# Kernel optimization log

Hardware: AMD Instinct MI355X
Metric: run time of the kernel (lower is better)

The kernel has to match this reference:

```python
import jax, jax.numpy as jnp
import numpy as np

N, D, H, E = 8192, 1024, 4096, 8


def setup_inputs() -> dict:
    key = jax.random.key(0)
    ks = jax.random.split(key, 5)
    s_in = 1.0 / np.sqrt(D)
    s_h = 1.0 / np.sqrt(H)
    return {
        "x": jax.random.normal(ks[0], (N, D), dtype=jnp.float32),
        "Wg": jax.random.normal(ks[1], (D, E), dtype=jnp.float32) * s_in,
        "bg": jnp.zeros((E,), dtype=jnp.float32),
        "W1": jax.random.normal(ks[2], (E, D, H), dtype=jnp.float32) * s_in,
        "b1": jnp.zeros((E, H), dtype=jnp.float32),
        "W2": jax.random.normal(ks[3], (E, H, D), dtype=jnp.float32) * s_h,
        "b2": jnp.zeros((E, D), dtype=jnp.float32),
    }


def reference(x, Wg, bg, W1, b1, W2, b2):
    # gate: softmax linear router -> weights [N, E]
    weights = jax.nn.softmax(x @ Wg + bg, axis=-1)
    # all experts, batched GEMMs: h [N, E, H]
    h = jax.nn.relu(jnp.einsum("nd,edh->neh", x, W1) + b1)  # Dropout is identity at inference
    outputs = jnp.einsum("neh,ehd->ned", h, W2) + b2         # [N, E, D]
    # weighted combine over experts
    return jnp.einsum("ne,ned->nd", weights, outputs)
```

## Files before the change

kernel.cpp:

```cpp
#include <hip/hip_runtime.h>
#include <hip/hip_bf16.h>

#define DDIM 1024
#define HDIM 4096
#define NEXP 8
#define NROW 8192

typedef __attribute__((ext_vector_type(8))) short s16x8;
typedef __attribute__((ext_vector_type(4))) float f32x4;

using bf16 = __hip_bfloat16;

__device__ __forceinline__ void gload16(const bf16* g, bf16* lds) {
    __builtin_amdgcn_global_load_lds(
        (const __attribute__((address_space(1))) unsigned int*)g,
        (__attribute__((address_space(3))) unsigned int*)lds,
        16, 0, 0);
}

template <int N>
__device__ __forceinline__ void wait_vmcnt() {
    if constexpr (N >= 6)      asm volatile("s_waitcnt vmcnt(6)" ::: "memory");
    else if constexpr (N == 3) asm volatile("s_waitcnt vmcnt(3)" ::: "memory");
    else                       asm volatile("s_waitcnt vmcnt(0)" ::: "memory");
}

__global__ void cvt_x_kernel(const float* __restrict__ x, bf16* __restrict__ xb, int total4) {
    int i = blockIdx.x * 256 + threadIdx.x;
    if (i >= total4) return;
    float4 v = ((const float4*)x)[i];
    union { bf16 b[4]; uint2 u; } p;
    p.b[0] = __float2bfloat16(v.x);
    p.b[1] = __float2bfloat16(v.y);
    p.b[2] = __float2bfloat16(v.z);
    p.b[3] = __float2bfloat16(v.w);
    ((uint2*)xb)[i] = p.u;
}

__global__ void transpose_cvt_kernel(const float* __restrict__ in, bf16* __restrict__ out,
                                     int R, int C) {
    __shared__ float tile[32][33];
    const size_t esz = (size_t)R * C;
    const float* src = in + (size_t)blockIdx.z * esz;
    bf16* dst = out + (size_t)blockIdx.z * esz;
    int c0 = blockIdx.x * 32, r0 = blockIdx.y * 32;
    int tx = threadIdx.x & 31, ty = threadIdx.x >> 5;
#pragma unroll
    for (int i = 0; i < 32; i += 8)
        tile[ty + i][tx] = src[(size_t)(r0 + ty + i) * C + (c0 + tx)];
    __syncthreads();
#pragma unroll
    for (int i = 0; i < 32; i += 8)
        dst[(size_t)(c0 + ty + i) * R + (r0 + tx)] = __float2bfloat16(tile[tx][ty + i]);
}

__global__ void gate_kernel(const float* __restrict__ x, const float* __restrict__ Wg,
                            const float* __restrict__ bg, float* __restrict__ wts) {
    int wave = threadIdx.x >> 6, lane = threadIdx.x & 63;
    int n = blockIdx.x * 4 + wave;
    const float* xr = x + (size_t)n * DDIM;
    float acc[NEXP] = {0.f, 0.f, 0.f, 0.f, 0.f, 0.f, 0.f, 0.f};
    for (int d = lane; d < DDIM; d += 64) {
        float xv = xr[d];
        const float* wr = Wg + (size_t)d * NEXP;
#pragma unroll
        for (int e = 0; e < NEXP; ++e) acc[e] += xv * wr[e];
    }
#pragma unroll
    for (int off = 32; off > 0; off >>= 1) {
#pragma unroll
        for (int e = 0; e < NEXP; ++e) acc[e] += __shfl_xor(acc[e], off, 64);
    }
    if (lane == 0) {
        float mx = -1e30f;
#pragma unroll
        for (int e = 0; e < NEXP; ++e) { acc[e] += bg[e]; mx = fmaxf(mx, acc[e]); }
        float s = 0.f;
#pragma unroll
        for (int e = 0; e < NEXP; ++e) { acc[e] = __expf(acc[e] - mx); s += acc[e]; }
        float inv = 1.0f / s;
#pragma unroll
        for (int e = 0; e < NEXP; ++e) wts[(size_t)n * NEXP + e] = acc[e] * inv;
    }
}

__global__ void out_init_kernel(const float* __restrict__ wts, const float* __restrict__ b2,
                                float* __restrict__ out) {
    size_t idx = (size_t)blockIdx.x * 256 + threadIdx.x;
    int d = (int)(idx & (DDIM - 1));
    size_t n = idx >> 10;
    const float* w = wts + n * NEXP;
    float s = 0.f;
#pragma unroll
    for (int e = 0; e < NEXP; ++e) s += w[e] * b2[(size_t)e * DDIM + d];
    out[idx] = s;
}

template <int MODE>
__global__ __launch_bounds__(512, 4) void gemm8(
    const bf16* __restrict__ A, const bf16* __restrict__ BT, void* __restrict__ Cout,
    const float* __restrict__ bias, const float* __restrict__ wts,
    int lda, int ldb, int ldc, int NT, int tilesM, int tilesN, int XGN, int expert) {
    constexpr int LPT = 3;
    constexpr int AELEMS = 256 * 32;
    constexpr int BELEMS = 128 * 32;
    __shared__ __align__(16) bf16 lds[3][AELEMS + BELEMS];

    const int tid = threadIdx.x;
    const int wave = tid >> 6, lane = tid & 63;
    const int wm = wave >> 2, wn = wave & 3;
    const int r = lane & 15, kg = lane >> 4;

    const int xcd = blockIdx.x & 7, slot = blockIdx.x >> 3;
    const int XGM = 8 / XGN;
    const int rm = tilesM / XGM, rn = tilesN / XGN;
    const int g = slot >> 5, u = slot & 31;
    const int gpr = rn >> 3;
    const int gm = (g / gpr) * 4 + (u >> 3);
    const int gn = (g % gpr) * 8 + (u & 7);
    const int tm = (xcd / XGN) * rm + gm;
    const int tn = (xcd % XGN) * rn + gn;

    const bf16* gA = A + (size_t)tm * 256 * lda;
    const bf16* gB = BT + (size_t)tn * 128 * ldb;

    f32x4 acc[8][2];
#pragma unroll
    for (int m = 0; m < 8; ++m)
#pragma unroll
        for (int n = 0; n < 2; ++n) acc[m][n] = (f32x4){0.f, 0.f, 0.f, 0.f};

    auto stageA = [&](int t) {
        bf16* Ab = lds[t % 3];
#pragma unroll
        for (int j = 0; j < 2; ++j) {
            int cw = (wave * 2 + j) * 64 + lane;
            int R = cw >> 2, kc = (cw & 3) ^ ((R >> 1) & 3);
            gload16(gA + (size_t)R * lda + t * 32 + kc * 8, Ab + (wave * 2 + j) * 512);
        }
    };
    auto stageB = [&](int t) {
        bf16* Bb = lds[t % 3] + AELEMS;
        int cw = wave * 64 + lane;
        int R = cw >> 2, kc = (cw & 3) ^ ((R >> 1) & 3);
        gload16(gB + (size_t)R * ldb + t * 32 + kc * 8, Bb + wave * 512);
    };

    stageA(0); stageB(0);
    stageA(1); stageB(1);
    wait_vmcnt<LPT>();
    __builtin_amdgcn_s_barrier();

    for (int t = 0; t < NT; ++t) {
        const bf16* Ab = lds[t % 3];
        const bf16* Bb = Ab + AELEMS;
        s16x8 afr[4], bfr[2];

#pragma unroll
        for (int n = 0; n < 2; ++n) {
            int R = wn * 32 + n * 16 + r;
            bfr[n] = *(const s16x8*)(Bb + R * 32 + ((kg ^ ((R >> 1) & 3)) * 8));
        }
#pragma unroll
        for (int m = 0; m < 4; ++m) {
            int R = wm * 128 + m * 16 + r;
            afr[m] = *(const s16x8*)(Ab + R * 32 + ((kg ^ ((R >> 1) & 3)) * 8));
        }
        if (t + 2 < NT) stageA(t + 2);
        __builtin_amdgcn_s_barrier();
        asm volatile("s_waitcnt lgkmcnt(0)" ::: "memory");
        __builtin_amdgcn_sched_barrier(0);
        __builtin_amdgcn_s_setprio(1);
#pragma unroll
        for (int m = 0; m < 4; ++m)
#pragma unroll
            for (int n = 0; n < 2; ++n)
                acc[m][n] = __builtin_amdgcn_mfma_f32_16x16x32_bf16(afr[m], bfr[n], acc[m][n], 0, 0, 0);
        __builtin_amdgcn_s_setprio(0);
        __builtin_amdgcn_s_barrier();

#pragma unroll
        for (int m = 0; m < 4; ++m) {
            int R = wm * 128 + (m + 4) * 16 + r;
            afr[m] = *(const s16x8*)(Ab + R * 32 + ((kg ^ ((R >> 1) & 3)) * 8));
        }
        if (t + 2 < NT) stageB(t + 2);
        __builtin_amdgcn_s_barrier();
        asm volatile("s_waitcnt lgkmcnt(0)" ::: "memory");
        __builtin_amdgcn_sched_barrier(0);
        __builtin_amdgcn_s_setprio(1);
#pragma unroll
        for (int m = 0; m < 4; ++m)
#pragma unroll
            for (int n = 0; n < 2; ++n)
                acc[m + 4][n] = __builtin_amdgcn_mfma_f32_16x16x32_bf16(afr[m], bfr[n], acc[m + 4][n], 0, 0, 0);
        __builtin_amdgcn_s_setprio(0);

        if (t + 1 < NT) {
            if (t + 2 < NT) wait_vmcnt<LPT>();
            else            wait_vmcnt<0>();
            __builtin_amdgcn_s_barrier();
        }
    }

    const size_t row0 = (size_t)tm * 256 + wm * 128;
    const int col0 = tn * 128 + wn * 32;
    if (MODE == 1) {
        bf16* H = (bf16*)Cout;
#pragma unroll
        for (int n = 0; n < 2; ++n) {
            int cc = col0 + n * 16 + r;
            float bv = bias[cc];
#pragma unroll
            for (int m = 0; m < 8; ++m) {
#pragma unroll
                for (int j = 0; j < 4; ++j) {
                    size_t rr = row0 + m * 16 + kg * 4 + j;
                    float v = acc[m][n][j] + bv;
                    v = v > 0.f ? v : 0.f;
                    H[rr * (size_t)ldc + cc] = __float2bfloat16(v);
                }
            }
        }
    } else {
        float* O = (float*)Cout;
#pragma unroll
        for (int m = 0; m < 8; ++m) {
#pragma unroll
            for (int j = 0; j < 4; ++j) {
                size_t rr = row0 + m * 16 + kg * 4 + j;
                float wv = wts[rr * NEXP + expert];
#pragma unroll
                for (int n = 0; n < 2; ++n) {
                    int cc = col0 + n * 16 + r;
                    O[rr * (size_t)ldc + cc] += wv * acc[m][n][j];
                }
            }
        }
    }
}

extern "C" void kernel_launch(void* const* d_in, const int* in_sizes, int n_in,
                              void* d_out, int out_size, void* d_ws, size_t ws_size,
                              hipStream_t stream) {
    const float* x  = (const float*)d_in[0];
    const float* Wg = (const float*)d_in[1];
    const float* bg = (const float*)d_in[2];
    const float* W1 = (const float*)d_in[3];
    const float* b1 = (const float*)d_in[4];
    const float* W2 = (const float*)d_in[5];
    const float* b2 = (const float*)d_in[6];
    float* out = (float*)d_out;

    char* ws = (char*)d_ws;
    bf16* xb   = (bf16*)(ws);
    bf16* W1T  = (bf16*)(ws + (16ull << 20));
    bf16* W2T  = (bf16*)(ws + (80ull << 20));
    bf16* Hb   = (bf16*)(ws + (144ull << 20));
    float* wts = (float*)(ws + (208ull << 20));

    cvt_x_kernel<<<(NROW * DDIM / 4 + 255) / 256, 256, 0, stream>>>(x, xb, NROW * DDIM / 4);
    transpose_cvt_kernel<<<dim3(HDIM / 32, DDIM / 32, NEXP), 256, 0, stream>>>(W1, W1T, DDIM, HDIM);
    transpose_cvt_kernel<<<dim3(DDIM / 32, HDIM / 32, NEXP), 256, 0, stream>>>(W2, W2T, HDIM, DDIM);
    gate_kernel<<<NROW / 4, 256, 0, stream>>>(x, Wg, bg, wts);
    out_init_kernel<<<NROW * DDIM / 256, 256, 0, stream>>>(wts, b2, out);

    for (int e = 0; e < NEXP; ++e) {
        gemm8<1><<<1024, 512, 0, stream>>>(
            xb, W1T + (size_t)e * HDIM * DDIM, Hb, b1 + (size_t)e * HDIM, nullptr,
            DDIM, DDIM, HDIM, DDIM / 32, 32, 32, 2, e);
        gemm8<2><<<256, 512, 0, stream>>>(
            Hb, W2T + (size_t)e * DDIM * HDIM, out, nullptr, wts,
            HDIM, HDIM, DDIM, HDIM / 32, 32, 8, 1, e);
    }
}
```

Baseline: 1.438 ms.

## Templatize GEMM tile width and rearrange waves to 4x2 layout

The GEMM kernel is templated on the number of 16-column subtiles per wave and on the number of compute phases. Waves now form a 4x2 grid, each owning 64 rows, instead of 2x4 with 128 rows each. The first GEMM uses a 256x256 tile (half the blocks, more B reuse per A load), and the second keeps 256x128 in a single phase. Launch bounds drop to 2 blocks per CU to allow more accumulator registers, at the cost of less occupancy and more LDS per block.

Measured after the change: 1.411 ms. Within noise of the previous version (-1.8%).

```diff
diff --git a/kernel.cpp b/kernel.cpp
--- a/kernel.cpp
+++ b/kernel.cpp
@@ -20,7 +20,7 @@
 
 template <int N>
 __device__ __forceinline__ void wait_vmcnt() {
-    if constexpr (N >= 6)      asm volatile("s_waitcnt vmcnt(6)" ::: "memory");
+    if constexpr (N == 4)      asm volatile("s_waitcnt vmcnt(4)" ::: "memory");
     else if constexpr (N == 3) asm volatile("s_waitcnt vmcnt(3)" ::: "memory");
     else                       asm volatile("s_waitcnt vmcnt(0)" ::: "memory");
 }
@@ -96,19 +96,22 @@
     out[idx] = s;
 }
 
-template <int MODE>
-__global__ __launch_bounds__(512, 4) void gemm8(
+template <int NR, int NPH, int MODE>
+__global__ __launch_bounds__(512, 2) void gemm8(
     const bf16* __restrict__ A, const bf16* __restrict__ BT, void* __restrict__ Cout,
     const float* __restrict__ bias, const float* __restrict__ wts,
     int lda, int ldb, int ldc, int NT, int tilesM, int tilesN, int XGN, int expert) {
-    constexpr int LPT = 3;
+    constexpr int BN = NR * 32;
+    constexpr int NRP = NR / NPH;
+    constexpr int BIN = BN / 128;
+    constexpr int LPT = 2 + BIN;
     constexpr int AELEMS = 256 * 32;
-    constexpr int BELEMS = 128 * 32;
+    constexpr int BELEMS = BN * 32;
     __shared__ __align__(16) bf16 lds[3][AELEMS + BELEMS];
 
     const int tid = threadIdx.x;
     const int wave = tid >> 6, lane = tid & 63;
-    const int wm = wave >> 2, wn = wave & 3;
+    const int wm = wave >> 1, wn = wave & 1;
     const int r = lane & 15, kg = lane >> 4;
 
     const int xcd = blockIdx.x & 7, slot = blockIdx.x >> 3;
@@ -122,28 +125,31 @@
     const int tn = (xcd % XGN) * rn + gn;
 
     const bf16* gA = A + (size_t)tm * 256 * lda;
-    const bf16* gB = BT + (size_t)tn * 128 * ldb;
-
-    f32x4 acc[8][2];
-#pragma unroll
-    for (int m = 0; m < 8; ++m)
-#pragma unroll
-        for (int n = 0; n < 2; ++n) acc[m][n] = (f32x4){0.f, 0.f, 0.f, 0.f};
+    const bf16* gB = BT + (size_t)tn * BN * ldb;
+
+    f32x4 acc[4][NR];
+#pragma unroll
+    for (int m = 0; m < 4; ++m)
+#pragma unroll
+        for (int n = 0; n < NR; ++n) acc[m][n] = (f32x4){0.f, 0.f, 0.f, 0.f};
 
     auto stageA = [&](int t) {
         bf16* Ab = lds[t % 3];
 #pragma unroll
         for (int j = 0; j < 2; ++j) {
-            int cw = (wave * 2 + j) * 64 + lane;
-            int R = cw >> 2, kc = (cw & 3) ^ ((R >> 1) & 3);
-            gload16(gA + (size_t)R * lda + t * 32 + kc * 8, Ab + (wave * 2 + j) * 512);
+            int c = j * 512 + tid;
+            int R = c >> 2, kc = (c & 3) ^ ((R >> 1) & 3);
+            gload16(gA + (size_t)R * lda + t * 32 + kc * 8, Ab + (j * 512 + wave * 64) * 8);
         }
     };
     auto stageB = [&](int t) {
         bf16* Bb = lds[t % 3] + AELEMS;
-        int cw = wave * 64 + lane;
-        int R = cw >> 2, kc = (cw & 3) ^ ((R >> 1) & 3);
-        gload16(gB + (size_t)R * ldb + t * 32 + kc * 8, Bb + wave * 512);
+#pragma unroll
+        for (int j = 0; j < BIN; ++j) {
+            int c = j * 512 + tid;
+            int R = c >> 2, kc = (c & 3) ^ ((R >> 1) & 3);
+            gload16(gB + (size_t)R * ldb + t * 32 + kc * 8, Bb + (j * 512 + wave * 64) * 8);
+        }
     };
 
     stageA(0); stageB(0);
@@ -154,19 +160,20 @@
     for (int t = 0; t < NT; ++t) {
         const bf16* Ab = lds[t % 3];
         const bf16* Bb = Ab + AELEMS;
-        s16x8 afr[4], bfr[2];
-
-#pragma unroll
-        for (int n = 0; n < 2; ++n) {
-            int R = wn * 32 + n * 16 + r;
+        s16x8 afr[4], bfr[NR];
+
+#pragma unroll
+        for (int m = 0; m < 4; ++m) {
+            int R = wm * 64 + m * 16 + r;
+            afr[m] = *(const s16x8*)(Ab + R * 32 + ((kg ^ ((R >> 1) & 3)) * 8));
+        }
+#pragma unroll
+        for (int n = 0; n < NRP; ++n) {
+            int R = wn * (NR * 16) + n * 16 + r;
             bfr[n] = *(const s16x8*)(Bb + R * 32 + ((kg ^ ((R >> 1) & 3)) * 8));
         }
-#pragma unroll
-        for (int m = 0; m < 4; ++m) {
-            int R = wm * 128 + m * 16 + r;
-            afr[m] = *(const s16x8*)(Ab + R * 32 + ((kg ^ ((R >> 1) & 3)) * 8));
-        }
         if (t + 2 < NT) stageA(t + 2);
+        if (NPH == 1 && t + 2 < NT) stageB(t + 2);
         __builtin_amdgcn_s_barrier();
         asm volatile("s_waitcnt lgkmcnt(0)" ::: "memory");
         __builtin_amdgcn_sched_barrier(0);
@@ -174,27 +181,29 @@
 #pragma unroll
         for (int m = 0; m < 4; ++m)
 #pragma unroll
-            for (int n = 0; n < 2; ++n)
+            for (int n = 0; n < NRP; ++n)
                 acc[m][n] = __builtin_amdgcn_mfma_f32_16x16x32_bf16(afr[m], bfr[n], acc[m][n], 0, 0, 0);
         __builtin_amdgcn_s_setprio(0);
-        __builtin_amdgcn_s_barrier();
-
-#pragma unroll
-        for (int m = 0; m < 4; ++m) {
-            int R = wm * 128 + (m + 4) * 16 + r;
-            afr[m] = *(const s16x8*)(Ab + R * 32 + ((kg ^ ((R >> 1) & 3)) * 8));
-        }
-        if (t + 2 < NT) stageB(t + 2);
-        __builtin_amdgcn_s_barrier();
-        asm volatile("s_waitcnt lgkmcnt(0)" ::: "memory");
-        __builtin_amdgcn_sched_barrier(0);
-        __builtin_amdgcn_s_setprio(1);
-#pragma unroll
-        for (int m = 0; m < 4; ++m)
-#pragma unroll
-            for (int n = 0; n < 2; ++n)
-                acc[m + 4][n] = __builtin_amdgcn_mfma_f32_16x16x32_bf16(afr[m], bfr[n], acc[m + 4][n], 0, 0, 0);
-        __builtin_amdgcn_s_setprio(0);
+
+        if (NPH == 2) {
+            __builtin_amdgcn_s_barrier();
+#pragma unroll
+            for (int n = NRP; n < NR; ++n) {
+                int R = wn * (NR * 16) + n * 16 + r;
+                bfr[n] = *(const s16x8*)(Bb + R * 32 + ((kg ^ ((R >> 1) & 3)) * 8));
+            }
+            if (t + 2 < NT) stageB(t + 2);
+            __builtin_amdgcn_s_barrier();
+            asm volatile("s_waitcnt lgkmcnt(0)" ::: "memory");
+            __builtin_amdgcn_sched_barrier(0);
+            __builtin_amdgcn_s_setprio(1);
+#pragma unroll
+            for (int m = 0; m < 4; ++m)
+#pragma unroll
+                for (int n = NRP; n < NR; ++n)
+                    acc[m][n] = __builtin_amdgcn_mfma_f32_16x16x32_bf16(afr[m], bfr[n], acc[m][n], 0, 0, 0);
+            __builtin_amdgcn_s_setprio(0);
+        }
 
         if (t + 1 < NT) {
             if (t + 2 < NT) wait_vmcnt<LPT>();
@@ -203,16 +212,16 @@
         }
     }
 
-    const size_t row0 = (size_t)tm * 256 + wm * 128;
-    const int col0 = tn * 128 + wn * 32;
+    const size_t row0 = (size_t)tm * 256 + wm * 64;
+    const int col0 = tn * BN + wn * (NR * 16);
     if (MODE == 1) {
         bf16* H = (bf16*)Cout;
 #pragma unroll
-        for (int n = 0; n < 2; ++n) {
+        for (int n = 0; n < NR; ++n) {
             int cc = col0 + n * 16 + r;
             float bv = bias[cc];
 #pragma unroll
-            for (int m = 0; m < 8; ++m) {
+            for (int m = 0; m < 4; ++m) {
 #pragma unroll
                 for (int j = 0; j < 4; ++j) {
                     size_t rr = row0 + m * 16 + kg * 4 + j;
@@ -225,13 +234,13 @@
     } else {
         float* O = (float*)Cout;
 #pragma unroll
-        for (int m = 0; m < 8; ++m) {
+        for (int m = 0; m < 4; ++m) {
 #pragma unroll
             for (int j = 0; j < 4; ++j) {
                 size_t rr = row0 + m * 16 + kg * 4 + j;
                 float wv = wts[rr * NEXP + expert];
 #pragma unroll
-                for (int n = 0; n < 2; ++n) {
+                for (int n = 0; n < NR; ++n) {
                     int cc = col0 + n * 16 + r;
                     O[rr * (size_t)ldc + cc] += wv * acc[m][n][j];
                 }
@@ -266,10 +275,10 @@
     out_init_kernel<<<NROW * DDIM / 256, 256, 0, stream>>>(wts, b2, out);
 
     for (int e = 0; e < NEXP; ++e) {
-        gemm8<1><<<1024, 512, 0, stream>>>(
+        gemm8<8, 2, 1><<<512, 512, 0, stream>>>(
             xb, W1T + (size_t)e * HDIM * DDIM, Hb, b1 + (size_t)e * HDIM, nullptr,
-            DDIM, DDIM, HDIM, DDIM / 32, 32, 32, 2, e);
-        gemm8<2><<<256, 512, 0, stream>>>(
+            DDIM, DDIM, HDIM, DDIM / 32, 32, 16, 2, e);
+        gemm8<4, 1, 2><<<256, 512, 0, stream>>>(
             Hb, W2T + (size_t)e * DDIM * HDIM, out, nullptr, wts,
             HDIM, HDIM, DDIM, HDIM / 32, 32, 8, 1, e);
     }
```
